# Optimization experiments

Measured on AMD Instinct MI355X. Metric: run time of the kernel, lower is better.

The kernel has to match this reference:

```python
import jax, jax.numpy as jnp
import numpy as np

N_NODES = 50000


def _gcn_norm(edge_index, n):
    # improved=True: self-loops with weight 2.0, sym normalization
    src, dst = edge_index[0], edge_index[1]
    loop = jnp.arange(n, dtype=src.dtype)
    src_f = jnp.concatenate([src, loop])
    dst_f = jnp.concatenate([dst, loop])
    ew = jnp.concatenate([jnp.ones(src.shape[0], jnp.float32),
                          jnp.full((n,), 2.0, jnp.float32)])
    deg = jax.ops.segment_sum(ew, dst_f, num_segments=n)
    dinv = jnp.where(deg > 0, jax.lax.rsqrt(deg), 0.0)
    norm = dinv[src_f] * ew * dinv[dst_f]
    return src_f, dst_f, norm


def _gcn_conv(x, W, b, src_f, dst_f, norm, n):
    h = x @ W  # [N, C_out]
    msg = h[src_f] * norm[:, None]  # gather + scale, [E+N, C_out]
    out = jax.ops.segment_sum(msg, dst_f, num_segments=n)  # scatter-add
    return out + b


def setup_inputs() -> dict:
    key = jax.random.key(0)
    ks = jax.random.split(key, 12)
    n, f_in, h, labels, e = N_NODES, 256, 128, 128, 800000
    s = 1.0 / np.sqrt(f_in)
    sh = 1.0 / np.sqrt(h)
    return {
        "x": jax.random.normal(ks[0], (n, f_in), jnp.float32),
        "edge_index": jax.random.randint(ks[1], (2, e), 0, n, jnp.int64),
        "W1": jax.random.uniform(ks[2], (f_in, h), jnp.float32, -s, s),
        "b1": jnp.zeros((h,), jnp.float32),
        "W2": jax.random.uniform(ks[3], (h, h), jnp.float32, -sh, sh),
        "b2": jnp.zeros((h,), jnp.float32),
        "We": jax.random.uniform(ks[4], (h, h), jnp.float32, -sh, sh),
        "be": jnp.zeros((h,), jnp.float32),
        "Wf": jax.random.uniform(ks[5], (h, labels), jnp.float32, -sh, sh),
        "bf": jax.random.uniform(ks[6], (labels,), jnp.float32, -sh, sh),
    }


def reference(x, edge_index, W1, b1, W2, b2, We, be, Wf, bf):
    n = x.shape[0]
    src_f, dst_f, norm = _gcn_norm(edge_index, n)
    h = jax.nn.relu(_gcn_conv(x, W1, b1, src_f, dst_f, norm, n))
    h = jax.nn.relu(_gcn_conv(h, W2, b2, src_f, dst_f, norm, n))
    h = _gcn_conv(h, We, be, src_f, dst_f, norm, n)
    return jax.nn.sigmoid(h @ Wf + bf)
```

## Files before the change

kernel.cpp:

```cpp
#include <hip/hip_runtime.h>
#include <stdint.h>

static constexpr int NN  = 50000;
static constexpr int EE  = 800000;
static constexpr int FIN = 256;
static constexpr int HID = 128;
static constexpr int SZ_LOG = 8;
static constexpr int NBUCK  = (NN + 255) >> SZ_LOG;
static constexpr int CH     = 2048;
static constexpr int NCBLK  = (EE + CH - 1) / CH;

typedef __attribute__((ext_vector_type(8))) short  short8;
typedef __attribute__((ext_vector_type(8))) __bf16 bf16x8;
typedef __attribute__((ext_vector_type(4))) float  f32x4;
typedef uint16_t u16;

__device__ __forceinline__ u16 f2bf(float f) {
  union { float f; uint32_t u; } v; v.f = f;
  return (u16)((v.u + 0x7fffu + ((v.u >> 16) & 1u)) >> 16);
}
__device__ __forceinline__ float bflo(uint32_t u) {
  union { uint32_t u; float f; } v; v.u = u << 16; return v.f;
}
__device__ __forceinline__ float bfhi(uint32_t u) {
  union { uint32_t u; float f; } v; v.u = u & 0xffff0000u; return v.f;
}
__device__ __forceinline__ void add8(float a[8], uint4 v) {
  a[0] += bflo(v.x); a[1] += bfhi(v.x);
  a[2] += bflo(v.y); a[3] += bfhi(v.y);
  a[4] += bflo(v.z); a[5] += bfhi(v.z);
  a[6] += bflo(v.w); a[7] += bfhi(v.w);
}

__global__ __launch_bounds__(256) void k_bhist(const int* __restrict__ dst, int* __restrict__ bcnt, int e) {
  __shared__ int lc[NBUCK];
  int tid = threadIdx.x;
  for (int i = tid; i < NBUCK; i += 256) lc[i] = 0;
  __syncthreads();
  int base = blockIdx.x * CH;
#pragma unroll
  for (int j = 0; j < 8; ++j) {
    int i = base + j * 256 + tid;
    if (i < e) atomicAdd(&lc[dst[i] >> SZ_LOG], 1);
  }
  __syncthreads();
  for (int i = tid; i < NBUCK; i += 256) if (lc[i]) atomicAdd(&bcnt[i], lc[i]);
}

__global__ __launch_bounds__(256) void k_bscan(const int* __restrict__ bcnt, int* __restrict__ boff,
                                               int* __restrict__ bcur, int* __restrict__ off) {
  __shared__ int buf[256];
  int tid = threadIdx.x;
  int v = (tid < NBUCK) ? bcnt[tid] : 0;
  buf[tid] = v;
  __syncthreads();
  for (int o = 1; o < 256; o <<= 1) {
    int t = (tid >= o) ? buf[tid - o] : 0;
    __syncthreads();
    buf[tid] += t;
    __syncthreads();
  }
  int ex = buf[tid] - v;
  if (tid < NBUCK) { boff[tid] = ex; bcur[tid] = ex; }
  if (tid == NBUCK - 1) boff[NBUCK] = ex + v;
  if (tid == 0) off[NN] = EE;
}

__global__ __launch_bounds__(256) void k_bscatter(const int* __restrict__ src, const int* __restrict__ dst,
                                                  int* __restrict__ bcur, int* __restrict__ ebuck, int e) {
  __shared__ int lc[NBUCK];
  __shared__ int lb[NBUCK];
  int tid = threadIdx.x;
  for (int i = tid; i < NBUCK; i += 256) lc[i] = 0;
  __syncthreads();
  int base = blockIdx.x * CH;
  int sj[8], dj[8], rj[8];
#pragma unroll
  for (int j = 0; j < 8; ++j) {
    int i = base + j * 256 + tid;
    if (i < e) {
      sj[j] = src[i]; dj[j] = dst[i];
      rj[j] = atomicAdd(&lc[dj[j] >> SZ_LOG], 1);
    }
  }
  __syncthreads();
  for (int i = tid; i < NBUCK; i += 256) { int c = lc[i]; if (c) lb[i] = atomicAdd(&bcur[i], c); }
  __syncthreads();
#pragma unroll
  for (int j = 0; j < 8; ++j) {
    int i = base + j * 256 + tid;
    if (i < e) ebuck[lb[dj[j] >> SZ_LOG] + rj[j]] = (sj[j] << 8) | (dj[j] & 255);
  }
}

__global__ __launch_bounds__(256) void k_ncount(const int* __restrict__ ebuck, const int* __restrict__ boff,
                                                int* __restrict__ off, float* __restrict__ dinv) {
  __shared__ int nc[256];
  __shared__ int sc[256];
  int b = blockIdx.x, tid = threadIdx.x;
  nc[tid] = 0;
  __syncthreads();
  int j0 = boff[b], j1 = boff[b + 1];
  for (int j = j0 + tid; j < j1; j += 256) atomicAdd(&nc[ebuck[j] & 255], 1);
  __syncthreads();
  int v = nc[tid];
  sc[tid] = v;
  __syncthreads();
  for (int o = 1; o < 256; o <<= 1) {
    int t = (tid >= o) ? sc[tid - o] : 0;
    __syncthreads();
    sc[tid] += t;
    __syncthreads();
  }
  int node = (b << SZ_LOG) + tid;
  if (node < NN) {
    off[node]  = j0 + sc[tid] - v;
    dinv[node] = rsqrtf((float)v + 2.0f);
  }
}

__global__ __launch_bounds__(256) void k_fill2(const int* __restrict__ ebuck, const int* __restrict__ boff,
                                               const int* __restrict__ off, int* __restrict__ edges) {
  __shared__ int lcur[256];
  int b = blockIdx.x, tid = threadIdx.x;
  int node = (b << SZ_LOG) + tid;
  lcur[tid] = (node < NN) ? off[node] : 0;
  __syncthreads();
  int j0 = boff[b], j1 = boff[b + 1];
  for (int j = j0 + tid; j < j1; j += 256) {
    int e = ebuck[j];
    int pos = atomicAdd(&lcur[e & 255], 1);
    edges[pos] = e >> 8;
  }
}

__global__ void k_wconv_all(const float* __restrict__ W1, const float* __restrict__ W2,
                            const float* __restrict__ We, const float* __restrict__ Wf,
                            u16* __restrict__ T1, u16* __restrict__ T2,
                            u16* __restrict__ T3, u16* __restrict__ T4) {
  int i = blockIdx.x * 256 + threadIdx.x;
  const float* W; u16* o;
  if (i < 32768)      { W = W1; o = T1; }
  else if (i < 49152) { W = W2; o = T2; i -= 32768; }
  else if (i < 65536) { W = We; o = T3; i -= 49152; }
  else                { W = Wf; o = T4; i -= 65536; }
  int k = i >> 7, c = i & 127;
  o[(size_t)((k >> 5) * 128 + c) * 32 + (k & 31)] = f2bf(W[i]);
}

template<int AFLOAT, int EPI>
__global__ __launch_bounds__(256) void k_gemm(const float* __restrict__ Af, const u16* __restrict__ Ah,
                                              const u16* __restrict__ Wt, const float* __restrict__ bias,
                                              const float* __restrict__ dinv,
                                              u16* __restrict__ gout, float* __restrict__ fout,
                                              int M, int K) {
  __shared__ u16 Ash[64 * 40];
  __shared__ u16 Bsh[128 * 40];
  const int tid  = threadIdx.x;
  const int lane = tid & 63;
  const int w    = tid >> 6;
  const int row0 = blockIdx.x * 64;
  f32x4 acc[8];
#pragma unroll
  for (int t = 0; t < 8; ++t) acc[t] = (f32x4){0.f, 0.f, 0.f, 0.f};

  const int nk = K >> 5;
  const int r = tid >> 2, kg = tid & 3;
  const int grow_a = row0 + r;
  for (int kb = 0; kb < nk; ++kb) {
    {
      int k0 = kb * 32 + kg * 8;
      alignas(16) u16 v[8];
      if (grow_a < M) {
        if (AFLOAT) {
          const float* p = Af + (size_t)grow_a * K + k0;
          float4 x0 = *(const float4*)(p);
          float4 x1 = *(const float4*)(p + 4);
          v[0] = f2bf(x0.x); v[1] = f2bf(x0.y); v[2] = f2bf(x0.z); v[3] = f2bf(x0.w);
          v[4] = f2bf(x1.x); v[5] = f2bf(x1.y); v[6] = f2bf(x1.z); v[7] = f2bf(x1.w);
        } else {
          *(uint4*)v = *(const uint4*)(Ah + (size_t)grow_a * K + k0);
        }
      } else {
#pragma unroll
        for (int i = 0; i < 8; ++i) v[i] = 0;
      }
      *(uint4*)&Ash[r * 40 + kg * 8] = *(const uint4*)v;
    }
    {
      const u16* wsrc = Wt + (size_t)kb * 4096;
#pragma unroll
      for (int j = 0; j < 2; ++j) {
        int chunk = tid * 2 + j;
        int rowb = chunk >> 2, kk = (chunk & 3) << 3;
        *(uint4*)&Bsh[rowb * 40 + kk] = *(const uint4*)(wsrc + chunk * 8);
      }
    }
    __syncthreads();
    {
      const int rl = lane & 15, kq = lane >> 4;
      short8 af = *(const short8*)&Ash[(w * 16 + rl) * 40 + kq * 8];
#pragma unroll
      for (int t = 0; t < 8; ++t) {
        short8 bf = *(const short8*)&Bsh[(t * 16 + rl) * 40 + kq * 8];
        acc[t] = __builtin_amdgcn_mfma_f32_16x16x32_bf16(
            __builtin_bit_cast(bf16x8, af), __builtin_bit_cast(bf16x8, bf), acc[t], 0, 0, 0);
      }
    }
    __syncthreads();
  }
  const int rl = lane & 15, rq = lane >> 4;
#pragma unroll
  for (int i = 0; i < 4; ++i) {
    int grow = row0 + w * 16 + rq * 4 + i;
    if (grow < M) {
      float dv = (EPI == 0) ? dinv[grow] : 0.f;
#pragma unroll
      for (int t = 0; t < 8; ++t) {
        int col = t * 16 + rl;
        if (EPI == 0) {
          gout[(size_t)grow * HID + col] = f2bf(dv * acc[t][i]);
        } else {
          float vv = acc[t][i] + bias[col];
          fout[(size_t)grow * HID + col] = 1.0f / (1.0f + __expf(-vv));
        }
      }
    }
  }
}

template<int RELU>
__global__ __launch_bounds__(256) void k_agg(const u16* __restrict__ h, u16* __restrict__ g,
                                             const float* __restrict__ bias, const float* __restrict__ dinv,
                                             const int* __restrict__ off, const int* __restrict__ edges,
                                             int n) {
  int wave = blockIdx.x * 4 + (threadIdx.x >> 6);
  int lane = threadIdx.x & 63;
  if (wave >= n) return;
  const int d  = wave;
  const int gr = lane >> 4;
  const int t  = lane & 15;
  const int c  = t << 3;
  float a[8];
#pragma unroll
  for (int i = 0; i < 8; ++i) a[i] = 0.f;

  int j  = off[d] + gr;
  const int j1 = off[d + 1];
  for (; j + 12 < j1; j += 16) {
    int s0 = edges[j], s1 = edges[j + 4], s2 = edges[j + 8], s3 = edges[j + 12];
    uint4 v0 = *(const uint4*)(h + (size_t)s0 * HID + c);
    uint4 v1 = *(const uint4*)(h + (size_t)s1 * HID + c);
    uint4 v2 = *(const uint4*)(h + (size_t)s2 * HID + c);
    uint4 v3 = *(const uint4*)(h + (size_t)s3 * HID + c);
    add8(a, v0); add8(a, v1); add8(a, v2); add8(a, v3);
  }
  for (; j + 4 < j1; j += 8) {
    int s0 = edges[j], s1 = edges[j + 4];
    uint4 v0 = *(const uint4*)(h + (size_t)s0 * HID + c);
    uint4 v1 = *(const uint4*)(h + (size_t)s1 * HID + c);
    add8(a, v0); add8(a, v1);
  }
  for (; j < j1; j += 4) {
    uint4 v0 = *(const uint4*)(h + (size_t)edges[j] * HID + c);
    add8(a, v0);
  }
#pragma unroll
  for (int i = 0; i < 8; ++i) {
    a[i] += __shfl_xor(a[i], 16);
    a[i] += __shfl_xor(a[i], 32);
  }
  float di = dinv[d];
  uint4 sv = *(const uint4*)(h + (size_t)d * HID + c);
  const float4 bv0 = *(const float4*)(bias + c);
  const float4 bv1 = *(const float4*)(bias + c + 4);
  a[0] = bv0.x + di * (a[0] + 2.f * bflo(sv.x));
  a[1] = bv0.y + di * (a[1] + 2.f * bfhi(sv.x));
  a[2] = bv0.z + di * (a[2] + 2.f * bflo(sv.y));
  a[3] = bv0.w + di * (a[3] + 2.f * bfhi(sv.y));
  a[4] = bv1.x + di * (a[4] + 2.f * bflo(sv.z));
  a[5] = bv1.y + di * (a[5] + 2.f * bfhi(sv.z));
  a[6] = bv1.z + di * (a[6] + 2.f * bflo(sv.w));
  a[7] = bv1.w + di * (a[7] + 2.f * bfhi(sv.w));
  if (RELU) {
#pragma unroll
    for (int i = 0; i < 8; ++i) a[i] = fmaxf(a[i], 0.f);
  }
  if (gr == 0) {
    uint4 o;
    o.x = (uint32_t)f2bf(a[0]) | ((uint32_t)f2bf(a[1]) << 16);
    o.y = (uint32_t)f2bf(a[2]) | ((uint32_t)f2bf(a[3]) << 16);
    o.z = (uint32_t)f2bf(a[4]) | ((uint32_t)f2bf(a[5]) << 16);
    o.w = (uint32_t)f2bf(a[6]) | ((uint32_t)f2bf(a[7]) << 16);
    *(uint4*)(g + (size_t)d * HID + c) = o;
  }
}

extern "C" void kernel_launch(void* const* d_in, const int* in_sizes, int n_in,
                              void* d_out, int out_size, void* d_ws, size_t ws_size,
                              hipStream_t stream) {
  const float* x   = (const float*)d_in[0];
  const int*   ei  = (const int*)d_in[1];
  const float* W1  = (const float*)d_in[2];
  const float* b1  = (const float*)d_in[3];
  const float* W2  = (const float*)d_in[4];
  const float* b2  = (const float*)d_in[5];
  const float* We  = (const float*)d_in[6];
  const float* be  = (const float*)d_in[7];
  const float* Wf  = (const float*)d_in[8];
  const float* bfv = (const float*)d_in[9];
  float* out = (float*)d_out;

  const int* src = ei;
  const int* dst = ei + EE;

  char* p = (char*)d_ws;
  auto take = [&](size_t bytes) { char* r = p; p += (bytes + 255) & ~(size_t)255; return r; };
  int*   bcnt  = (int*)take((size_t)NBUCK * 4);
  int*   boff  = (int*)take((size_t)(NBUCK + 1) * 4);
  int*   bcur  = (int*)take((size_t)NBUCK * 4);
  int*   off   = (int*)take((size_t)(NN + 1) * 4);
  float* dinv  = (float*)take((size_t)NN * 4);
  int*   edges = (int*)take((size_t)EE * 4);
  u16*   hA    = (u16*)take((size_t)NN * HID * 2);
  u16*   hB    = (u16*)take((size_t)NN * HID * 2);
  u16*   Wt1   = (u16*)take((size_t)FIN * HID * 2);
  u16*   Wt2   = (u16*)take((size_t)HID * HID * 2);
  u16*   Wt3   = (u16*)take((size_t)HID * HID * 2);
  u16*   Wt4   = (u16*)take((size_t)HID * HID * 2);
  int*   ebuck = (int*)hB;

  hipMemsetAsync(bcnt, 0, (size_t)NBUCK * 4, stream);
  k_bhist<<<NCBLK, 256, 0, stream>>>(dst, bcnt, EE);
  k_bscan<<<1, 256, 0, stream>>>(bcnt, boff, bcur, off);
  k_bscatter<<<NCBLK, 256, 0, stream>>>(src, dst, bcur, ebuck, EE);
  k_ncount<<<NBUCK, 256, 0, stream>>>(ebuck, boff, off, dinv);
  k_fill2<<<NBUCK, 256, 0, stream>>>(ebuck, boff, off, edges);

  k_wconv_all<<<(81920 + 255) / 256, 256, 0, stream>>>(W1, W2, We, Wf, Wt1, Wt2, Wt3, Wt4);

  const int gemm_grid = (NN + 63) / 64;
  const int agg_grid  = (NN + 3) / 4;

  k_gemm<1, 0><<<gemm_grid, 256, 0, stream>>>(x, nullptr, Wt1, nullptr, dinv, hA, nullptr, NN, FIN);
  k_agg<1><<<agg_grid, 256, 0, stream>>>(hA, hB, b1, dinv, off, edges, NN);
  k_gemm<0, 0><<<gemm_grid, 256, 0, stream>>>(nullptr, hB, Wt2, nullptr, dinv, hA, nullptr, NN, HID);
  k_agg<1><<<agg_grid, 256, 0, stream>>>(hA, hB, b2, dinv, off, edges, NN);
  k_gemm<0, 0><<<gemm_grid, 256, 0, stream>>>(nullptr, hB, Wt3, nullptr, dinv, hA, nullptr, NN, HID);
  k_agg<0><<<agg_grid, 256, 0, stream>>>(hA, hB, be, dinv, off, edges, NN);
  k_gemm<0, 1><<<gemm_grid, 256, 0, stream>>>(nullptr, hB, Wt4, bfv, dinv, nullptr, out, NN, HID);
}
```

Measured before the change: 293.7 us.

## Fuse node count and edge fill kernels; double GEMM row tile to 128

```diff
diff --git a/kernel.cpp b/kernel.cpp
--- a/kernel.cpp
+++ b/kernel.cpp
@@ -93,10 +93,12 @@
   }
 }
 
-__global__ __launch_bounds__(256) void k_ncount(const int* __restrict__ ebuck, const int* __restrict__ boff,
-                                                int* __restrict__ off, float* __restrict__ dinv) {
+__global__ __launch_bounds__(256) void k_nfill(const int* __restrict__ ebuck, const int* __restrict__ boff,
+                                               int* __restrict__ off, float* __restrict__ dinv,
+                                               int* __restrict__ edges) {
   __shared__ int nc[256];
   __shared__ int sc[256];
+  __shared__ int lcur[256];
   int b = blockIdx.x, tid = threadIdx.x;
   nc[tid] = 0;
   __syncthreads();
@@ -112,21 +114,14 @@
     sc[tid] += t;
     __syncthreads();
   }
+  int ex = j0 + sc[tid] - v;
+  lcur[tid] = ex;
   int node = (b << SZ_LOG) + tid;
   if (node < NN) {
-    off[node]  = j0 + sc[tid] - v;
+    off[node]  = ex;
     dinv[node] = rsqrtf((float)v + 2.0f);
   }
-}
-
-__global__ __launch_bounds__(256) void k_fill2(const int* __restrict__ ebuck, const int* __restrict__ boff,
-                                               const int* __restrict__ off, int* __restrict__ edges) {
-  __shared__ int lcur[256];
-  int b = blockIdx.x, tid = threadIdx.x;
-  int node = (b << SZ_LOG) + tid;
-  lcur[tid] = (node < NN) ? off[node] : 0;
-  __syncthreads();
-  int j0 = boff[b], j1 = boff[b + 1];
+  __syncthreads();
   for (int j = j0 + tid; j < j1; j += 256) {
     int e = ebuck[j];
     int pos = atomicAdd(&lcur[e & 255], 1);
@@ -154,38 +149,46 @@
                                               const float* __restrict__ dinv,
                                               u16* __restrict__ gout, float* __restrict__ fout,
                                               int M, int K) {
-  __shared__ u16 Ash[64 * 40];
+  __shared__ u16 Ash[128 * 40];
   __shared__ u16 Bsh[128 * 40];
   const int tid  = threadIdx.x;
   const int lane = tid & 63;
   const int w    = tid >> 6;
-  const int row0 = blockIdx.x * 64;
-  f32x4 acc[8];
-#pragma unroll
-  for (int t = 0; t < 8; ++t) acc[t] = (f32x4){0.f, 0.f, 0.f, 0.f};
+  const int row0 = blockIdx.x * 128;
+  f32x4 acc0[8], acc1[8];
+#pragma unroll
+  for (int t = 0; t < 8; ++t) { acc0[t] = (f32x4){0.f,0.f,0.f,0.f}; acc1[t] = (f32x4){0.f,0.f,0.f,0.f}; }
 
   const int nk = K >> 5;
-  const int r = tid >> 2, kg = tid & 3;
+  const int r = tid >> 1, half = tid & 1;
   const int grow_a = row0 + r;
+  const bool aok = (grow_a < M);
   for (int kb = 0; kb < nk; ++kb) {
     {
-      int k0 = kb * 32 + kg * 8;
-      alignas(16) u16 v[8];
-      if (grow_a < M) {
+      int k0 = kb * 32 + half * 16;
+      alignas(16) u16 v[16];
+      if (aok) {
         if (AFLOAT) {
           const float* p = Af + (size_t)grow_a * K + k0;
           float4 x0 = *(const float4*)(p);
           float4 x1 = *(const float4*)(p + 4);
-          v[0] = f2bf(x0.x); v[1] = f2bf(x0.y); v[2] = f2bf(x0.z); v[3] = f2bf(x0.w);
-          v[4] = f2bf(x1.x); v[5] = f2bf(x1.y); v[6] = f2bf(x1.z); v[7] = f2bf(x1.w);
+          float4 x2 = *(const float4*)(p + 8);
+          float4 x3 = *(const float4*)(p + 12);
+          v[0]  = f2bf(x0.x); v[1]  = f2bf(x0.y); v[2]  = f2bf(x0.z); v[3]  = f2bf(x0.w);
+          v[4]  = f2bf(x1.x); v[5]  = f2bf(x1.y); v[6]  = f2bf(x1.z); v[7]  = f2bf(x1.w);
+          v[8]  = f2bf(x2.x); v[9]  = f2bf(x2.y); v[10] = f2bf(x2.z); v[11] = f2bf(x2.w);
+          v[12] = f2bf(x3.x); v[13] = f2bf(x3.y); v[14] = f2bf(x3.z); v[15] = f2bf(x3.w);
         } else {
-          *(uint4*)v = *(const uint4*)(Ah + (size_t)grow_a * K + k0);
+          const u16* p = Ah + (size_t)grow_a * K + k0;
+          *(uint4*)v       = *(const uint4*)(p);
+          *(uint4*)(v + 8) = *(const uint4*)(p + 8);
         }
       } else {
 #pragma unroll
-        for (int i = 0; i < 8; ++i) v[i] = 0;
+        for (int i = 0; i < 16; ++i) v[i] = 0;
       }
-      *(uint4*)&Ash[r * 40 + kg * 8] = *(const uint4*)v;
+      *(uint4*)&Ash[r * 40 + half * 16]     = *(const uint4*)v;
+      *(uint4*)&Ash[r * 40 + half * 16 + 8] = *(const uint4*)(v + 8);
     }
     {
       const u16* wsrc = Wt + (size_t)kb * 4096;
@@ -199,30 +202,37 @@
     __syncthreads();
     {
       const int rl = lane & 15, kq = lane >> 4;
-      short8 af = *(const short8*)&Ash[(w * 16 + rl) * 40 + kq * 8];
+      short8 af0 = *(const short8*)&Ash[(w * 16 + rl) * 40 + kq * 8];
+      short8 af1 = *(const short8*)&Ash[(64 + w * 16 + rl) * 40 + kq * 8];
 #pragma unroll
       for (int t = 0; t < 8; ++t) {
         short8 bf = *(const short8*)&Bsh[(t * 16 + rl) * 40 + kq * 8];
-        acc[t] = __builtin_amdgcn_mfma_f32_16x16x32_bf16(
-            __builtin_bit_cast(bf16x8, af), __builtin_bit_cast(bf16x8, bf), acc[t], 0, 0, 0);
+        acc0[t] = __builtin_amdgcn_mfma_f32_16x16x32_bf16(
+            __builtin_bit_cast(bf16x8, af0), __builtin_bit_cast(bf16x8, bf), acc0[t], 0, 0, 0);
+        acc1[t] = __builtin_amdgcn_mfma_f32_16x16x32_bf16(
+            __builtin_bit_cast(bf16x8, af1), __builtin_bit_cast(bf16x8, bf), acc1[t], 0, 0, 0);
       }
     }
     __syncthreads();
   }
   const int rl = lane & 15, rq = lane >> 4;
 #pragma unroll
-  for (int i = 0; i < 4; ++i) {
-    int grow = row0 + w * 16 + rq * 4 + i;
-    if (grow < M) {
-      float dv = (EPI == 0) ? dinv[grow] : 0.f;
-#pragma unroll
-      for (int t = 0; t < 8; ++t) {
-        int col = t * 16 + rl;
-        if (EPI == 0) {
-          gout[(size_t)grow * HID + col] = f2bf(dv * acc[t][i]);
-        } else {
-          float vv = acc[t][i] + bias[col];
-          fout[(size_t)grow * HID + col] = 1.0f / (1.0f + __expf(-vv));
+  for (int h2 = 0; h2 < 2; ++h2) {
+#pragma unroll
+    for (int i = 0; i < 4; ++i) {
+      int grow = row0 + h2 * 64 + w * 16 + rq * 4 + i;
+      if (grow < M) {
+        float dv = (EPI == 0) ? dinv[grow] : 0.f;
+#pragma unroll
+        for (int t = 0; t < 8; ++t) {
+          int col = t * 16 + rl;
+          float av = h2 ? acc1[t][i] : acc0[t][i];
+          if (EPI == 0) {
+            gout[(size_t)grow * HID + col] = f2bf(dv * av);
+          } else {
+            float vv = av + bias[col];
+            fout[(size_t)grow * HID + col] = 1.0f / (1.0f + __expf(-vv));
+          }
         }
       }
     }
@@ -334,12 +344,11 @@
   k_bhist<<<NCBLK, 256, 0, stream>>>(dst, bcnt, EE);
   k_bscan<<<1, 256, 0, stream>>>(bcnt, boff, bcur, off);
   k_bscatter<<<NCBLK, 256, 0, stream>>>(src, dst, bcur, ebuck, EE);
-  k_ncount<<<NBUCK, 256, 0, stream>>>(ebuck, boff, off, dinv);
-  k_fill2<<<NBUCK, 256, 0, stream>>>(ebuck, boff, off, edges);
+  k_nfill<<<NBUCK, 256, 0, stream>>>(ebuck, boff, off, dinv, edges);
 
   k_wconv_all<<<(81920 + 255) / 256, 256, 0, stream>>>(W1, W2, We, Wf, Wt1, Wt2, Wt3, Wt4);
 
-  const int gemm_grid = (NN + 63) / 64;
+  const int gemm_grid = (NN + 127) / 128;
   const int agg_grid  = (NN + 3) / 4;
 
   k_gemm<1, 0><<<gemm_grid, 256, 0, stream>>>(x, nullptr, Wt1, nullptr, dinv, hA, nullptr, NN, FIN);
```

Result: no change. 299.5 us (+2.0%).
